# Kernel optimization log

Measured on AMD Instinct MI355X. Metric: run time of the kernel, lower is better.

The kernel has to match this reference:

```python
import jax, jax.numpy as jnp
import numpy as np

EPS = 1e-6

def ln_fwd(x, gamma, beta):
    # gamma/beta broadcast shape [1,H,1,D]
    mu = x.mean(axis=-1, keepdims=True)
    var = ((x - mu) ** 2).mean(axis=-1, keepdims=True)
    x_hat = (x - mu) / jnp.sqrt(var + EPS)
    return gamma * x_hat + beta

def ln_fused_l2_bwd(x, residual, pred, gamma, beta):
    # grad wrt x of || (gamma*ln(x)+beta) + residual - pred ||^2 (fused form)
    mu = x.mean(axis=-1, keepdims=True)
    var = ((x - mu) ** 2).mean(axis=-1, keepdims=True)
    std = jnp.sqrt(var + EPS)
    x_hat = (x - mu) / std
    y = gamma * x_hat + beta + residual
    grad_output = 2.0 * (y - pred)
    gxh = grad_output * gamma
    z = (gxh - gxh.mean(axis=-1, keepdims=True)
         - x_hat * (gxh * x_hat).mean(axis=-1, keepdims=True)) / std
    return z

def _combine(a, b):
    # a precedes b in sequence; recurrence x[t] = g[t]*x[t-1] + u[t]
    ga, ua = a
    gb, ub = b
    return (ga * gb, gb * ua + ub)

def setup_inputs() -> dict:
    key = jax.random.key(0)
    ks = jax.random.split(key, 8)
    B, H, L, D = 1, 16, 2048, 64
    q = jax.random.normal(ks[0], (B, H, L, D), dtype=jnp.float32)
    k = jax.random.normal(ks[1], (B, H, L, D), dtype=jnp.float32)
    v = jax.random.normal(ks[2], (B, H, L, D), dtype=jnp.float32)
    gate = jax.random.uniform(ks[3], (B, H, L), dtype=jnp.float32)
    eta = jax.random.uniform(ks[4], (B, H, L), dtype=jnp.float32) * 0.1
    W0 = jax.random.normal(ks[5], (H, D, D), dtype=jnp.float32) / jnp.sqrt(jnp.float32(D))
    gamma = jnp.ones((H, 1, D), dtype=jnp.float32)
    beta = jnp.zeros((H, 1, D), dtype=jnp.float32)
    return {"q": q, "k": k, "v": v, "gate": gate, "eta": eta,
            "W0": W0, "gamma": gamma, "beta": beta}

def reference(q, k, v, gate, eta, W0, gamma, beta):
    # q,k,v: [B,H,L,D]; gate,eta: [B,H,L]; W0: [H,D,D]; gamma,beta: [H,1,D]
    g = gamma[None]          # [1,H,1,D]
    b = beta[None]
    # inner-loop TTT gradient at initial fast weights W0
    Z1 = jnp.einsum('bhld,hde->bhle', k, W0)                  # [B,H,L,D]
    grad_l = ln_fused_l2_bwd(Z1, k, v, g, b)                  # [B,H,L,D]
    # per-token fast-weight update: -eta[t] * outer(k[t], grad_l[t])
    token = -eta[..., None, None] * (k[..., :, None] * grad_l[..., None, :])  # [B,H,L,D,D]
    gates = gate[..., None, None]                             # [B,H,L,1,1]
    # gated linear recurrence W[t] = gate[t]*W[t-1] + token[t] via associative scan
    gc, uc = jax.lax.associative_scan(_combine, (gates, token), axis=2)
    W = uc + gc * W0[None, :, None]                           # [B,H,L,D,D]
    # readout with post-LN and residual
    Zq = jnp.einsum('bhld,bhlde->bhle', q, W)                 # [B,H,L,D]
    out = ln_fwd(Zq, g, b) + q
    return out
```

## Files before the change

### kernel.cpp

```cpp
#include <hip/hip_runtime.h>
#include <hip/hip_bf16.h>
#include <math.h>


#define H 16
#define L 2048
#define D 64
#define C 64
#define NC 32

typedef short s8v __attribute__((ext_vector_type(8)));
typedef short s4v __attribute__((ext_vector_type(4)));
typedef float f4v __attribute__((ext_vector_type(4)));

__device__ inline unsigned short f2bf(float x) {
  unsigned u = __float_as_uint(x);
  return (unsigned short)((u + 0x7fffu + ((u >> 16) & 1u)) >> 16);
}
__device__ inline float bf2f(unsigned short s) { return __uint_as_float(((unsigned)s) << 16); }

__device__ inline int swz(int row, int colByte) { return row * 128 + (colByte ^ ((row & 7) << 4)); }

__device__ inline s8v ld8(const short* base, int row, int colByte) {
  return *(const s8v*)((const char*)base + swz(row, colByte));
}
__device__ inline void st4(short* base, int row, int colByte, s4v v) {
  *(s4v*)((char*)base + swz(row, colByte)) = v;
}
__device__ inline void st2(short* base, int row, int colByte, unsigned v) {
  *(unsigned*)((char*)base + swz(row, colByte)) = v;
}
__device__ inline void st1(short* base, int row, int colByte, unsigned short v) {
  *(short*)((char*)base + swz(row, colByte)) = (short)v;
}

__device__ inline void red16(float& x) {
  x += __shfl_xor(x, 1, 64);
  x += __shfl_xor(x, 2, 64);
  x += __shfl_xor(x, 4, 64);
  x += __shfl_xor(x, 8, 64);
}

__device__ inline f4v MM(s8v a, s8v b, f4v c) {
  return __builtin_amdgcn_mfma_f32_16x16x32_bf16(a, b, c, 0, 0, 0);
}

__device__ inline f4v MM3(s8v ah, s8v al, s8v bh, s8v bl, f4v c) {
  c = MM(ah, bh, c);
  c = MM(ah, bl, c);
  c = MM(al, bh, c);
  return c;
}

__global__ __launch_bounds__(256, 2) void k_chunk(
    const float4* __restrict__ Q4, const float4* __restrict__ K4,
    const float* __restrict__ Kg, const float* __restrict__ Vg,
    const float* __restrict__ gate, const float* __restrict__ eta,
    const float4* __restrict__ W04, const float* __restrict__ gamma,
    const float* __restrict__ beta,
    float* __restrict__ Ut, float* __restrict__ Pg, float* __restrict__ Out)
{
  __shared__ __align__(16) short Khi[4096];
  __shared__ __align__(16) short Klo[4096];
  __shared__ __align__(16) short KtH[4096];
  __shared__ __align__(16) short KtL[4096];
  __shared__ __align__(16) short W0h[4096];
  __shared__ __align__(16) short W0l[4096];
  __shared__ float cl[64], wj[64];

  int tid = threadIdx.x;
  int h = blockIdx.x >> 5, c = blockIdx.x & 31;
  int rowb = h * L + c * C;
  int R = tid >> 6, l = tid & 63, g = l >> 4, c16 = l & 15;
  int arow = 16 * R + c16;
  int kb0 = 16 * g, kb1 = 64 + 16 * g;

  const float4* qp = Q4 + (size_t)(rowb + arow) * 16;
  float4 qA0 = qp[2 * g], qA1 = qp[2 * g + 1], qA2 = qp[8 + 2 * g], qA3 = qp[8 + 2 * g + 1];
  float kk[4][4], vv[4][4], er[4];
  #pragma unroll
  for (int r = 0; r < 4; ++r) {
    int jr = 16 * R + 4 * g + r;
    const float* kp = Kg + (size_t)(rowb + jr) * 64 + c16;
    const float* vp = Vg + (size_t)(rowb + jr) * 64 + c16;
    #pragma unroll
    for (int ct = 0; ct < 4; ++ct) {
      kk[r][ct] = kp[16 * ct];
      vv[r][ct] = vp[16 * ct];
    }
    er[r] = eta[rowb + jr];
  }

  {
    float x = logf(fmaxf(gate[rowb + l], 1e-37f));
    #pragma unroll
    for (int off = 1; off < 64; off <<= 1) {
      float n = __shfl_up(x, off, 64);
      if (l >= off) x += n;
    }
    cl[l] = x;
    float c63 = __shfl(x, 63, 64);
    wj[l] = expf(c63 - x);
    if (R == 0) Pg[rowb + l] = expf(x);
  }

  #pragma unroll
  for (int it = 0; it < 2; ++it) {
    int idx = tid + it * 256;
    int rp = idx >> 4, g4 = idx & 15;
    int j0 = 2 * rp, j1 = j0 + 1;
    float4 k0 = K4[(size_t)(rowb + j0) * 16 + g4];
    float4 k1 = K4[(size_t)(rowb + j1) * 16 + g4];
    float4 w0 = W04[(size_t)h * 1024 + j0 * 16 + g4];
    float4 w1 = W04[(size_t)h * 1024 + j1 * 16 + g4];
    float w0j = wj[j0], w1j = wj[j1];
    float ke0[4] = {k0.x, k0.y, k0.z, k0.w};
    float ke1[4] = {k1.x, k1.y, k1.z, k1.w};
    float we0[4] = {w0.x, w0.y, w0.z, w0.w};
    float we1[4] = {w1.x, w1.y, w1.z, w1.w};
    s4v kh0, kl0, kh1, kl1;
    #pragma unroll
    for (int e = 0; e < 4; ++e) {
      unsigned short hb0 = f2bf(ke0[e]);
      kh0[e] = (short)hb0; kl0[e] = (short)f2bf(ke0[e] - bf2f(hb0));
      unsigned short hb1 = f2bf(ke1[e]);
      kh1[e] = (short)hb1; kl1[e] = (short)f2bf(ke1[e] - bf2f(hb1));
      int dr = 4 * g4 + e;
      float wk0 = ke0[e] * w0j, wk1 = ke1[e] * w1j;
      unsigned short th0 = f2bf(wk0), th1 = f2bf(wk1);
      st2(KtH, dr, 2 * j0, (unsigned)th0 | ((unsigned)th1 << 16));
      st2(KtL, dr, 2 * j0,
          (unsigned)f2bf(wk0 - bf2f(th0)) | ((unsigned)f2bf(wk1 - bf2f(th1)) << 16));
      unsigned short wh0 = f2bf(we0[e]), wh1 = f2bf(we1[e]);
      st2(W0h, dr, 2 * j0, (unsigned)wh0 | ((unsigned)wh1 << 16));
      st2(W0l, dr, 2 * j0,
          (unsigned)f2bf(we0[e] - bf2f(wh0)) | ((unsigned)f2bf(we1[e] - bf2f(wh1)) << 16));
    }
    st4(Khi, j0, 8 * g4, kh0); st4(Klo, j0, 8 * g4, kl0);
    st4(Khi, j1, 8 * g4, kh1); st4(Klo, j1, 8 * g4, kl1);
  }

  s8v aQh0, aQl0, aQh1, aQl1;
  {
    float q0[8] = {qA0.x, qA0.y, qA0.z, qA0.w, qA1.x, qA1.y, qA1.z, qA1.w};
    float q1[8] = {qA2.x, qA2.y, qA2.z, qA2.w, qA3.x, qA3.y, qA3.z, qA3.w};
    #pragma unroll
    for (int e = 0; e < 8; ++e) {
      unsigned short hb = f2bf(q0[e]);
      aQh0[e] = (short)hb; aQl0[e] = (short)f2bf(q0[e] - bf2f(hb));
      unsigned short hb1 = f2bf(q1[e]);
      aQh1[e] = (short)hb1; aQl1[e] = (short)f2bf(q1[e] - bf2f(hb1));
    }
  }
  __syncthreads();

  f4v accS[4];
  #pragma unroll
  for (int ct = 0; ct < 4; ++ct) {
    int br = 16 * ct + c16;
    f4v a = {0.f, 0.f, 0.f, 0.f};
    a = MM3(aQh0, aQl0, ld8(Khi, br, kb0), ld8(Klo, br, kb0), a);
    a = MM3(aQh1, aQl1, ld8(Khi, br, kb1), ld8(Klo, br, kb1), a);
    accS[ct] = a;
  }

  s8v aKh0 = ld8(Khi, arow, kb0), aKh1 = ld8(Khi, arow, kb1);
  s8v aKl0 = ld8(Klo, arow, kb0), aKl1 = ld8(Klo, arow, kb1);
  f4v accZ[4];
  #pragma unroll
  for (int ct = 0; ct < 4; ++ct) {
    int br = 16 * ct + c16;
    f4v a = {0.f, 0.f, 0.f, 0.f};
    a = MM3(aKh0, aKl0, ld8(W0h, br, kb0), ld8(W0l, br, kb0), a);
    a = MM3(aKh1, aKl1, ld8(W0h, br, kb1), ld8(W0l, br, kb1), a);
    accZ[ct] = a;
  }

  float ga[4], be[4];
  #pragma unroll
  for (int ct = 0; ct < 4; ++ct) {
    ga[ct] = gamma[h * 64 + 16 * ct + c16];
    be[ct] = beta[h * 64 + 16 * ct + c16];
  }
  float gtreg[4][4];
  #pragma unroll
  for (int r = 0; r < 4; ++r) {
    float s1 = accZ[0][r] + accZ[1][r] + accZ[2][r] + accZ[3][r];
    red16(s1);
    float mu = s1 * (1.f / 64.f);
    float dv[4], s2 = 0.f;
    #pragma unroll
    for (int ct = 0; ct < 4; ++ct) { dv[ct] = accZ[ct][r] - mu; s2 += dv[ct] * dv[ct]; }
    red16(s2);
    float rstd = rsqrtf(s2 * (1.f / 64.f) + 1e-6f);
    float xh[4], gxh[4], t1 = 0.f, t2 = 0.f;
    #pragma unroll
    for (int ct = 0; ct < 4; ++ct) {
      xh[ct] = dv[ct] * rstd;
      float go = 2.f * (fmaf(ga[ct], xh[ct], be[ct]) + kk[r][ct] - vv[r][ct]);
      gxh[ct] = go * ga[ct];
      t1 += gxh[ct];
      t2 += gxh[ct] * xh[ct];
    }
    red16(t1);
    red16(t2);
    float m1 = t1 * (1.f / 64.f), m2 = t2 * (1.f / 64.f);
    #pragma unroll
    for (int ct = 0; ct < 4; ++ct)
      gtreg[r][ct] = -er[r] * (gxh[ct] - m1 - xh[ct] * m2) * rstd;
  }
  __syncthreads();

  #pragma unroll
  for (int ct = 0; ct < 4; ++ct) {
    s4v gh, gl;
    #pragma unroll
    for (int r = 0; r < 4; ++r) {
      unsigned short hb = f2bf(gtreg[r][ct]);
      gh[r] = (short)hb;
      gl[r] = (short)f2bf(gtreg[r][ct] - bf2f(hb));
    }
    st4(W0h, 16 * ct + c16, 2 * (16 * R + 4 * g), gh);
    st4(W0l, 16 * ct + c16, 2 * (16 * R + 4 * g), gl);
  }
  float cli[4];
  #pragma unroll
  for (int r = 0; r < 4; ++r) cli[r] = cl[16 * R + 4 * g + r];
  #pragma unroll
  for (int ct = 0; ct < 4; ++ct) {
    int j = 16 * ct + c16;
    float clj = cl[j];
    #pragma unroll
    for (int r = 0; r < 4; ++r) {
      int i = 16 * R + 4 * g + r;
      float s = (j <= i) ? accS[ct][r] * expf(cli[r] - clj) : 0.f;
      unsigned short hb = f2bf(s);
      st1(Khi, i, 2 * j, hb);
      st1(Klo, i, 2 * j, f2bf(s - bf2f(hb)));
    }
  }
  __syncthreads();

  s8v aSh0 = ld8(Khi, arow, kb0), aSh1 = ld8(Khi, arow, kb1);
  s8v aSl0 = ld8(Klo, arow, kb0), aSl1 = ld8(Klo, arow, kb1);
  #pragma unroll
  for (int ct = 0; ct < 4; ++ct) {
    int br = 16 * ct + c16;
    f4v a = {0.f, 0.f, 0.f, 0.f};
    a = MM3(aSh0, aSl0, ld8(W0h, br, kb0), ld8(W0l, br, kb0), a);
    a = MM3(aSh1, aSl1, ld8(W0h, br, kb1), ld8(W0l, br, kb1), a);
    #pragma unroll
    for (int r = 0; r < 4; ++r)
      Out[(size_t)(rowb + 16 * R + 4 * g + r) * 64 + 16 * ct + c16] = a[r];
  }

  float* ub = Ut + (size_t)(h * NC + c) * 4096;
  s8v aGh0 = ld8(W0h, arow, kb0), aGh1 = ld8(W0h, arow, kb1);
  s8v aGl0 = ld8(W0l, arow, kb0), aGl1 = ld8(W0l, arow, kb1);
  #pragma unroll
  for (int ct = 0; ct < 4; ++ct) {
    int br = 16 * ct + c16;
    f4v a = {0.f, 0.f, 0.f, 0.f};
    a = MM3(aGh0, aGl0, ld8(KtH, br, kb0), ld8(KtL, br, kb0), a);
    a = MM3(aGh1, aGl1, ld8(KtH, br, kb1), ld8(KtL, br, kb1), a);
    #pragma unroll
    for (int r = 0; r < 4; ++r)
      ub[(16 * R + 4 * g + r) * 64 + 16 * ct + c16] = a[r];
  }
}

__global__ __launch_bounds__(256) void k_scan(
    const float* __restrict__ W0, const float* __restrict__ Ut,
    const float* __restrict__ Pg, float* __restrict__ Wpt)
{
  int t = blockIdx.x * 256 + threadIdx.x;
  int h = t >> 12;
  int idx = t & 4095;
  int erow = idx >> 6, d = idx & 63;
  float w = W0[h * 4096 + d * 64 + erow];
  #pragma unroll
  for (int c2 = 0; c2 < NC; ++c2) {
    int off = (h * NC + c2) * 4096 + idx;
    Wpt[off] = w;
    w = fmaf(Pg[h * L + c2 * 64 + 63], w, Ut[off]);
  }
}

__global__ __launch_bounds__(256, 2) void k_out(
    const float4* __restrict__ Q4, const float* __restrict__ Qg,
    const float4* __restrict__ Wpt4, const float* __restrict__ Pg,
    const float* __restrict__ gamma, const float* __restrict__ beta,
    float* __restrict__ Out)
{
  __shared__ __align__(16) short Whi[4096];
  __shared__ __align__(16) short Wlo[4096];
  int tid = threadIdx.x;
  int h = blockIdx.x >> 5, c = blockIdx.x & 31;
  int rowb = h * L + c * C;
  int R = tid >> 6, l = tid & 63, g = l >> 4, c16 = l & 15;
  int arow = 16 * R + c16;
  int kb0 = 16 * g, kb1 = 64 + 16 * g;

  const float4* qp = Q4 + (size_t)(rowb + arow) * 16;
  float4 qA0 = qp[2 * g], qA1 = qp[2 * g + 1], qA2 = qp[8 + 2 * g], qA3 = qp[8 + 2 * g + 1];
  float io[4][4], qres[4][4], pr[4];
  #pragma unroll
  for (int r = 0; r < 4; ++r) {
    int row = rowb + 16 * R + 4 * g + r;
    pr[r] = Pg[row];
    #pragma unroll
    for (int ct = 0; ct < 4; ++ct) {
      io[r][ct] = Out[(size_t)row * 64 + 16 * ct + c16];
      qres[r][ct] = Qg[(size_t)row * 64 + 16 * ct + c16];
    }
  }

  for (int idx = tid; idx < 1024; idx += 256) {
    int row = idx >> 4, g4 = idx & 15;
    float4 wv = Wpt4[(size_t)(h * NC + c) * 1024 + idx];
    float we[4] = {wv.x, wv.y, wv.z, wv.w};
    s4v wh, wl;
    #pragma unroll
    for (int e = 0; e < 4; ++e) {
      unsigned short hb = f2bf(we[e]);
      wh[e] = (short)hb;
      wl[e] = (short)f2bf(we[e] - bf2f(hb));
    }
    st4(Whi, row, 8 * g4, wh);
    st4(Wlo, row, 8 * g4, wl);
  }

  s8v ah0, al0, ah1, al1;
  {
    float q0[8] = {qA0.x, qA0.y, qA0.z, qA0.w, qA1.x, qA1.y, qA1.z, qA1.w};
    float q1[8] = {qA2.x, qA2.y, qA2.z, qA2.w, qA3.x, qA3.y, qA3.z, qA3.w};
    #pragma unroll
    for (int e = 0; e < 8; ++e) {
      unsigned short hb = f2bf(q0[e]);
      ah0[e] = (short)hb; al0[e] = (short)f2bf(q0[e] - bf2f(hb));
      unsigned short hb1 = f2bf(q1[e]);
      ah1[e] = (short)hb1; al1[e] = (short)f2bf(q1[e] - bf2f(hb1));
    }
  }
  __syncthreads();

  f4v acc[4];
  #pragma unroll
  for (int ct = 0; ct < 4; ++ct) {
    int br = 16 * ct + c16;
    f4v a = {0.f, 0.f, 0.f, 0.f};
    a = MM3(ah0, al0, ld8(Whi, br, kb0), ld8(Wlo, br, kb0), a);
    a = MM3(ah1, al1, ld8(Whi, br, kb1), ld8(Wlo, br, kb1), a);
    acc[ct] = a;
  }
  float ga[4], be[4];
  #pragma unroll
  for (int ct = 0; ct < 4; ++ct) {
    ga[ct] = gamma[h * 64 + 16 * ct + c16];
    be[ct] = beta[h * 64 + 16 * ct + c16];
  }
  #pragma unroll
  for (int r = 0; r < 4; ++r) {
    int row = rowb + 16 * R + 4 * g + r;
    float zq[4];
    #pragma unroll
    for (int ct = 0; ct < 4; ++ct)
      zq[ct] = fmaf(pr[r], acc[ct][r], io[r][ct]);
    float s1 = zq[0] + zq[1] + zq[2] + zq[3];
    red16(s1);
    float mu = s1 * (1.f / 64.f);
    float dv[4], s2 = 0.f;
    #pragma unroll
    for (int ct = 0; ct < 4; ++ct) { dv[ct] = zq[ct] - mu; s2 += dv[ct] * dv[ct]; }
    red16(s2);
    float rstd = rsqrtf(s2 * (1.f / 64.f) + 1e-6f);
    #pragma unroll
    for (int ct = 0; ct < 4; ++ct) {
      float o = fmaf(ga[ct], dv[ct] * rstd, be[ct]) + qres[r][ct];
      Out[(size_t)row * 64 + 16 * ct + c16] = o;
    }
  }
}

extern "C" void kernel_launch(void* const* d_in, const int* in_sizes, int n_in,
                              void* d_out, int out_size, void* d_ws, size_t ws_size,
                              hipStream_t stream) {
  const float* q     = (const float*)d_in[0];
  const float* k     = (const float*)d_in[1];
  const float* v     = (const float*)d_in[2];
  const float* gate  = (const float*)d_in[3];
  const float* eta   = (const float*)d_in[4];
  const float* W0    = (const float*)d_in[5];
  const float* gamma = (const float*)d_in[6];
  const float* beta  = (const float*)d_in[7];
  float* out = (float*)d_out;
  float* ws  = (float*)d_ws;

  float* Pg  = ws;
  float* Ut  = ws + 32768;
  float* Wpt = ws + 32768 + 2097152;

  k_chunk<<<H * NC, 256, 0, stream>>>(
      (const float4*)q, (const float4*)k, k, v, gate, eta,
      (const float4*)W0, gamma, beta, Ut, Pg, out);
  k_scan<<<256, 256, 0, stream>>>(W0, Ut, Pg, Wpt);
  k_out<<<H * NC, 256, 0, stream>>>(
      (const float4*)q, q, (const float4*)Wpt, Pg, gamma, beta, out);
}
```

Measured before the change: 31.87 us.

## Fuse chunk-state scan into chunk kernel via last-block atomic counter

Removes the separate k_scan launch. Each chunk block now increments a per-head atomic counter, and the last block for a head runs the sequential inter-chunk scan over Ut using float4 accesses. It also moves the decay weighting from the K^T operand onto the gradient operand, which needs extra LDS buffers, and issues the K/W0 global loads earlier. The trade is one fewer kernel launch against a memset launch, a serialized scan done by only 16 blocks (one per head), and higher LDS use that may reduce occupancy.

```diff
diff --git a/kernel.cpp b/kernel.cpp
--- a/kernel.cpp
+++ b/kernel.cpp
@@ -6,7 +6,6 @@
 #define H 16
 #define L 2048
 #define D 64
-#define C 64
 #define NC 32
 
 typedef short s8v __attribute__((ext_vector_type(8)));
@@ -44,7 +43,6 @@
 __device__ inline f4v MM(s8v a, s8v b, f4v c) {
   return __builtin_amdgcn_mfma_f32_16x16x32_bf16(a, b, c, 0, 0, 0);
 }
-
 __device__ inline f4v MM3(s8v ah, s8v al, s8v bh, s8v bl, f4v c) {
   c = MM(ah, bh, c);
   c = MM(ah, bl, c);
@@ -57,8 +55,9 @@
     const float* __restrict__ Kg, const float* __restrict__ Vg,
     const float* __restrict__ gate, const float* __restrict__ eta,
     const float4* __restrict__ W04, const float* __restrict__ gamma,
-    const float* __restrict__ beta,
-    float* __restrict__ Ut, float* __restrict__ Pg, float* __restrict__ Out)
+    const float* __restrict__ beta, const float* __restrict__ W0f,
+    float* __restrict__ Ut, float* __restrict__ Pg, float* __restrict__ Gc,
+    float* __restrict__ Wpt, int* __restrict__ Cnt, float* __restrict__ Out)
 {
   __shared__ __align__(16) short Khi[4096];
   __shared__ __align__(16) short Klo[4096];
@@ -66,14 +65,31 @@
   __shared__ __align__(16) short KtL[4096];
   __shared__ __align__(16) short W0h[4096];
   __shared__ __align__(16) short W0l[4096];
-  __shared__ float cl[64], wj[64];
+  __shared__ __align__(16) short GwH[4096];
+  __shared__ __align__(16) short GwL[4096];
+  __shared__ float cl[64];
+  __shared__ int lastFlag;
 
   int tid = threadIdx.x;
-  int h = blockIdx.x >> 5, c = blockIdx.x & 31;
-  int rowb = h * L + c * C;
+  int bid = blockIdx.x;
+  int h = bid >> 5;
+  int rowb = h * L + (bid & 31) * 64;
   int R = tid >> 6, l = tid & 63, g = l >> 4, c16 = l & 15;
   int arow = 16 * R + c16;
   int kb0 = 16 * g, kb1 = 64 + 16 * g;
+
+  float gv = gate[rowb + l];
+
+  int g4 = tid & 15;
+  float4 kA[2][2], wA[2][2];
+  #pragma unroll
+  for (int it = 0; it < 2; ++it) {
+    int j0 = 2 * ((tid >> 4) + it * 16);
+    kA[it][0] = K4[(size_t)(rowb + j0) * 16 + g4];
+    kA[it][1] = K4[(size_t)(rowb + j0 + 1) * 16 + g4];
+    wA[it][0] = W04[(size_t)h * 1024 + j0 * 16 + g4];
+    wA[it][1] = W04[(size_t)h * 1024 + (j0 + 1) * 16 + g4];
+  }
 
   const float4* qp = Q4 + (size_t)(rowb + arow) * 16;
   float4 qA0 = qp[2 * g], qA1 = qp[2 * g + 1], qA2 = qp[8 + 2 * g], qA3 = qp[8 + 2 * g + 1];
@@ -91,53 +107,46 @@
     er[r] = eta[rowb + jr];
   }
 
+  float c63v;
   {
-    float x = logf(fmaxf(gate[rowb + l], 1e-37f));
+    float x = logf(fmaxf(gv, 1e-37f));
     #pragma unroll
     for (int off = 1; off < 64; off <<= 1) {
       float n = __shfl_up(x, off, 64);
       if (l >= off) x += n;
     }
     cl[l] = x;
-    float c63 = __shfl(x, 63, 64);
-    wj[l] = expf(c63 - x);
+    c63v = __shfl(x, 63, 64);
     if (R == 0) Pg[rowb + l] = expf(x);
+    if (tid == 63) Gc[bid] = expf(x);
   }
 
   #pragma unroll
   for (int it = 0; it < 2; ++it) {
-    int idx = tid + it * 256;
-    int rp = idx >> 4, g4 = idx & 15;
-    int j0 = 2 * rp, j1 = j0 + 1;
-    float4 k0 = K4[(size_t)(rowb + j0) * 16 + g4];
-    float4 k1 = K4[(size_t)(rowb + j1) * 16 + g4];
-    float4 w0 = W04[(size_t)h * 1024 + j0 * 16 + g4];
-    float4 w1 = W04[(size_t)h * 1024 + j1 * 16 + g4];
-    float w0j = wj[j0], w1j = wj[j1];
-    float ke0[4] = {k0.x, k0.y, k0.z, k0.w};
-    float ke1[4] = {k1.x, k1.y, k1.z, k1.w};
-    float we0[4] = {w0.x, w0.y, w0.z, w0.w};
-    float we1[4] = {w1.x, w1.y, w1.z, w1.w};
+    int j0 = 2 * ((tid >> 4) + it * 16);
+    float ke0[4] = {kA[it][0].x, kA[it][0].y, kA[it][0].z, kA[it][0].w};
+    float ke1[4] = {kA[it][1].x, kA[it][1].y, kA[it][1].z, kA[it][1].w};
+    float we0[4] = {wA[it][0].x, wA[it][0].y, wA[it][0].z, wA[it][0].w};
+    float we1[4] = {wA[it][1].x, wA[it][1].y, wA[it][1].z, wA[it][1].w};
     s4v kh0, kl0, kh1, kl1;
     #pragma unroll
     for (int e = 0; e < 4; ++e) {
       unsigned short hb0 = f2bf(ke0[e]);
-      kh0[e] = (short)hb0; kl0[e] = (short)f2bf(ke0[e] - bf2f(hb0));
+      unsigned short lb0 = f2bf(ke0[e] - bf2f(hb0));
       unsigned short hb1 = f2bf(ke1[e]);
-      kh1[e] = (short)hb1; kl1[e] = (short)f2bf(ke1[e] - bf2f(hb1));
+      unsigned short lb1 = f2bf(ke1[e] - bf2f(hb1));
+      kh0[e] = (short)hb0; kl0[e] = (short)lb0;
+      kh1[e] = (short)hb1; kl1[e] = (short)lb1;
       int dr = 4 * g4 + e;
-      float wk0 = ke0[e] * w0j, wk1 = ke1[e] * w1j;
-      unsigned short th0 = f2bf(wk0), th1 = f2bf(wk1);
-      st2(KtH, dr, 2 * j0, (unsigned)th0 | ((unsigned)th1 << 16));
-      st2(KtL, dr, 2 * j0,
-          (unsigned)f2bf(wk0 - bf2f(th0)) | ((unsigned)f2bf(wk1 - bf2f(th1)) << 16));
+      st2(KtH, dr, 2 * j0, (unsigned)hb0 | ((unsigned)hb1 << 16));
+      st2(KtL, dr, 2 * j0, (unsigned)lb0 | ((unsigned)lb1 << 16));
       unsigned short wh0 = f2bf(we0[e]), wh1 = f2bf(we1[e]);
       st2(W0h, dr, 2 * j0, (unsigned)wh0 | ((unsigned)wh1 << 16));
       st2(W0l, dr, 2 * j0,
           (unsigned)f2bf(we0[e] - bf2f(wh0)) | ((unsigned)f2bf(we1[e] - bf2f(wh1)) << 16));
     }
     st4(Khi, j0, 8 * g4, kh0); st4(Klo, j0, 8 * g4, kl0);
-    st4(Khi, j1, 8 * g4, kh1); st4(Klo, j1, 8 * g4, kl1);
+    st4(Khi, j0 + 1, 8 * g4, kh1); st4(Klo, j0 + 1, 8 * g4, kl1);
   }
 
   s8v aQh0, aQl0, aQh1, aQl1;
@@ -181,6 +190,12 @@
   for (int ct = 0; ct < 4; ++ct) {
     ga[ct] = gamma[h * 64 + 16 * ct + c16];
     be[ct] = beta[h * 64 + 16 * ct + c16];
+  }
+  float cli[4], wjr[4];
+  #pragma unroll
+  for (int r = 0; r < 4; ++r) {
+    cli[r] = cl[16 * R + 4 * g + r];
+    wjr[r] = expf(c63v - cli[r]);
   }
   float gtreg[4][4];
   #pragma unroll
@@ -213,19 +228,22 @@
 
   #pragma unroll
   for (int ct = 0; ct < 4; ++ct) {
-    s4v gh, gl;
+    s4v gh, gl, uh, ul;
     #pragma unroll
     for (int r = 0; r < 4; ++r) {
-      unsigned short hb = f2bf(gtreg[r][ct]);
+      float gtv = gtreg[r][ct];
+      unsigned short hb = f2bf(gtv);
       gh[r] = (short)hb;
-      gl[r] = (short)f2bf(gtreg[r][ct] - bf2f(hb));
-    }
-    st4(W0h, 16 * ct + c16, 2 * (16 * R + 4 * g), gh);
-    st4(W0l, 16 * ct + c16, 2 * (16 * R + 4 * g), gl);
-  }
-  float cli[4];
-  #pragma unroll
-  for (int r = 0; r < 4; ++r) cli[r] = cl[16 * R + 4 * g + r];
+      gl[r] = (short)f2bf(gtv - bf2f(hb));
+      float gw = gtv * wjr[r];
+      unsigned short hb2 = f2bf(gw);
+      uh[r] = (short)hb2;
+      ul[r] = (short)f2bf(gw - bf2f(hb2));
+    }
+    int er2 = 16 * ct + c16, cb = 2 * (16 * R + 4 * g);
+    st4(W0h, er2, cb, gh); st4(W0l, er2, cb, gl);
+    st4(GwH, er2, cb, uh); st4(GwL, er2, cb, ul);
+  }
   #pragma unroll
   for (int ct = 0; ct < 4; ++ct) {
     int j = 16 * ct + c16;
@@ -254,9 +272,9 @@
       Out[(size_t)(rowb + 16 * R + 4 * g + r) * 64 + 16 * ct + c16] = a[r];
   }
 
-  float* ub = Ut + (size_t)(h * NC + c) * 4096;
-  s8v aGh0 = ld8(W0h, arow, kb0), aGh1 = ld8(W0h, arow, kb1);
-  s8v aGl0 = ld8(W0l, arow, kb0), aGl1 = ld8(W0l, arow, kb1);
+  float* ub = Ut + (size_t)bid * 4096;
+  s8v aGh0 = ld8(GwH, arow, kb0), aGh1 = ld8(GwH, arow, kb1);
+  s8v aGl0 = ld8(GwL, arow, kb0), aGl1 = ld8(GwL, arow, kb1);
   #pragma unroll
   for (int ct = 0; ct < 4; ++ct) {
     int br = 16 * ct + c16;
@@ -267,22 +285,42 @@
     for (int r = 0; r < 4; ++r)
       ub[(16 * R + 4 * g + r) * 64 + 16 * ct + c16] = a[r];
   }
-}
-
-__global__ __launch_bounds__(256) void k_scan(
-    const float* __restrict__ W0, const float* __restrict__ Ut,
-    const float* __restrict__ Pg, float* __restrict__ Wpt)
-{
-  int t = blockIdx.x * 256 + threadIdx.x;
-  int h = t >> 12;
-  int idx = t & 4095;
-  int erow = idx >> 6, d = idx & 63;
-  float w = W0[h * 4096 + d * 64 + erow];
-  #pragma unroll
-  for (int c2 = 0; c2 < NC; ++c2) {
-    int off = (h * NC + c2) * 4096 + idx;
-    Wpt[off] = w;
-    w = fmaf(Pg[h * L + c2 * 64 + 63], w, Ut[off]);
+
+  __syncthreads();
+  if (tid == 0) {
+    __threadfence();
+    lastFlag = (atomicAdd(&Cnt[h], 1) == NC - 1) ? 1 : 0;
+  }
+  __syncthreads();
+  if (lastFlag) {
+    __threadfence();
+    const float4* ut4 = (const float4*)Ut + (size_t)h * NC * 1024;
+    float4* wp4 = (float4*)Wpt + (size_t)h * NC * 1024;
+    const float* gcp = Gc + h * NC;
+    float4 w[4];
+    #pragma unroll
+    for (int j = 0; j < 4; ++j) {
+      int e4 = tid + j * 256;
+      int erow = e4 >> 4, d0 = (e4 & 15) * 4;
+      const float* w0p = W0f + (size_t)h * 4096 + erow;
+      w[j].x = w0p[(d0 + 0) * 64];
+      w[j].y = w0p[(d0 + 1) * 64];
+      w[j].z = w0p[(d0 + 2) * 64];
+      w[j].w = w0p[(d0 + 3) * 64];
+    }
+    for (int c2 = 0; c2 < NC; ++c2) {
+      float gcv = gcp[c2];
+      #pragma unroll
+      for (int j = 0; j < 4; ++j) {
+        size_t off = (size_t)c2 * 1024 + tid + j * 256;
+        wp4[off] = w[j];
+        float4 u = ut4[off];
+        w[j].x = fmaf(gcv, w[j].x, u.x);
+        w[j].y = fmaf(gcv, w[j].y, u.y);
+        w[j].z = fmaf(gcv, w[j].z, u.z);
+        w[j].w = fmaf(gcv, w[j].w, u.w);
+      }
+    }
   }
 }
 
@@ -296,7 +334,7 @@
   __shared__ __align__(16) short Wlo[4096];
   int tid = threadIdx.x;
   int h = blockIdx.x >> 5, c = blockIdx.x & 31;
-  int rowb = h * L + c * C;
+  int rowb = h * L + c * 64;
   int R = tid >> 6, l = tid & 63, g = l >> 4, c16 = l & 15;
   int arow = 16 * R + c16;
   int kb0 = 16 * g, kb1 = 64 + 16 * g;
@@ -397,13 +435,16 @@
   float* ws  = (float*)d_ws;
 
   float* Pg  = ws;
-  float* Ut  = ws + 32768;
-  float* Wpt = ws + 32768 + 2097152;
-
+  float* Gc  = ws + 32768;
+  float* Ut  = ws + 33280;
+  float* Wpt = ws + 33280 + 2097152;
+  int*   Cnt = (int*)(ws + 33280 + 2 * 2097152);
+
+  hipMemsetAsync(Cnt, 0, H * sizeof(int), stream);
   k_chunk<<<H * NC, 256, 0, stream>>>(
       (const float4*)q, (const float4*)k, k, v, gate, eta,
-      (const float4*)W0, gamma, beta, Ut, Pg, out);
-  k_scan<<<256, 256, 0, stream>>>(W0, Ut, Pg, Wpt);
+      (const float4*)W0, gamma, beta, W0,
+      Ut, Pg, Gc, Wpt, Cnt, out);
   k_out<<<H * NC, 256, 0, stream>>>(
       (const float4*)q, q, (const float4*)Wpt, Pg, gamma, beta, out);
 }
```

Result: slower. 78.20 us (+145.4%).

## Split chunk and output kernels across 8 waves with column-halved tiles

Applied to the files above, without the earlier changes.

Doubles the block size of k_chunk and k_out to 512 threads. Each pair of waves splits the 64 output columns, and the row statistics for the layer norms are exchanged through shared memory. The decay weighting now multiplies the gradient tile into separate GwH/GwL buffers instead of scaling K during staging, and the variance uses E[x^2]-mu^2 in a single pass. The aim is more waves in flight and shorter per-wave dependency chains, at the cost of extra barriers, more LDS, and a slightly less stable variance formula.

```diff
diff --git a/kernel.cpp b/kernel.cpp
--- a/kernel.cpp
+++ b/kernel.cpp
@@ -6,7 +6,6 @@
 #define H 16
 #define L 2048
 #define D 64
-#define C 64
 #define NC 32
 
 typedef short s8v __attribute__((ext_vector_type(8)));
@@ -44,7 +43,6 @@
 __device__ inline f4v MM(s8v a, s8v b, f4v c) {
   return __builtin_amdgcn_mfma_f32_16x16x32_bf16(a, b, c, 0, 0, 0);
 }
-
 __device__ inline f4v MM3(s8v ah, s8v al, s8v bh, s8v bl, f4v c) {
   c = MM(ah, bh, c);
   c = MM(ah, bl, c);
@@ -52,7 +50,7 @@
   return c;
 }
 
-__global__ __launch_bounds__(256, 2) void k_chunk(
+__global__ __launch_bounds__(512, 4) void k_chunk(
     const float4* __restrict__ Q4, const float4* __restrict__ K4,
     const float* __restrict__ Kg, const float* __restrict__ Vg,
     const float* __restrict__ gate, const float* __restrict__ eta,
@@ -66,71 +64,75 @@
   __shared__ __align__(16) short KtL[4096];
   __shared__ __align__(16) short W0h[4096];
   __shared__ __align__(16) short W0l[4096];
-  __shared__ float cl[64], wj[64];
+  __shared__ __align__(16) short GwH[4096];
+  __shared__ __align__(16) short GwL[4096];
+  __shared__ float cl[64];
+  __shared__ float exA[2][64], exB[2][64], exC[2][64], exD[2][64];
 
   int tid = threadIdx.x;
-  int h = blockIdx.x >> 5, c = blockIdx.x & 31;
-  int rowb = h * L + c * C;
-  int R = tid >> 6, l = tid & 63, g = l >> 4, c16 = l & 15;
-  int arow = 16 * R + c16;
+  int h = blockIdx.x >> 5;
+  int rowb = h * L + (blockIdx.x & 31) * 64;
+  int w = tid >> 6, l = tid & 63;
+  int RG = w >> 1, CH = w & 1;
+  int g = l >> 4, c16 = l & 15;
+  int arow = 16 * RG + c16;
   int kb0 = 16 * g, kb1 = 64 + 16 * g;
+
+  float gv = gate[rowb + l];
+
+  int pairI = tid >> 4, g4 = tid & 15;
+  int j0 = 2 * pairI, j1 = j0 + 1;
+  float4 kA0 = K4[(size_t)(rowb + j0) * 16 + g4];
+  float4 kA1 = K4[(size_t)(rowb + j1) * 16 + g4];
+  float4 wA0 = W04[(size_t)h * 1024 + j0 * 16 + g4];
+  float4 wA1 = W04[(size_t)h * 1024 + j1 * 16 + g4];
 
   const float4* qp = Q4 + (size_t)(rowb + arow) * 16;
   float4 qA0 = qp[2 * g], qA1 = qp[2 * g + 1], qA2 = qp[8 + 2 * g], qA3 = qp[8 + 2 * g + 1];
-  float kk[4][4], vv[4][4], er[4];
-  #pragma unroll
-  for (int r = 0; r < 4; ++r) {
-    int jr = 16 * R + 4 * g + r;
+  float kk[4][2], vv[4][2], er[4];
+  #pragma unroll
+  for (int r = 0; r < 4; ++r) {
+    int jr = 16 * RG + 4 * g + r;
     const float* kp = Kg + (size_t)(rowb + jr) * 64 + c16;
     const float* vp = Vg + (size_t)(rowb + jr) * 64 + c16;
     #pragma unroll
-    for (int ct = 0; ct < 4; ++ct) {
-      kk[r][ct] = kp[16 * ct];
-      vv[r][ct] = vp[16 * ct];
+    for (int j = 0; j < 2; ++j) {
+      kk[r][j] = kp[16 * (2 * CH + j)];
+      vv[r][j] = vp[16 * (2 * CH + j)];
     }
     er[r] = eta[rowb + jr];
   }
 
+  float c63v;
   {
-    float x = logf(fmaxf(gate[rowb + l], 1e-37f));
+    float x = logf(fmaxf(gv, 1e-37f));
     #pragma unroll
     for (int off = 1; off < 64; off <<= 1) {
       float n = __shfl_up(x, off, 64);
       if (l >= off) x += n;
     }
     cl[l] = x;
-    float c63 = __shfl(x, 63, 64);
-    wj[l] = expf(c63 - x);
-    if (R == 0) Pg[rowb + l] = expf(x);
-  }
-
-  #pragma unroll
-  for (int it = 0; it < 2; ++it) {
-    int idx = tid + it * 256;
-    int rp = idx >> 4, g4 = idx & 15;
-    int j0 = 2 * rp, j1 = j0 + 1;
-    float4 k0 = K4[(size_t)(rowb + j0) * 16 + g4];
-    float4 k1 = K4[(size_t)(rowb + j1) * 16 + g4];
-    float4 w0 = W04[(size_t)h * 1024 + j0 * 16 + g4];
-    float4 w1 = W04[(size_t)h * 1024 + j1 * 16 + g4];
-    float w0j = wj[j0], w1j = wj[j1];
-    float ke0[4] = {k0.x, k0.y, k0.z, k0.w};
-    float ke1[4] = {k1.x, k1.y, k1.z, k1.w};
-    float we0[4] = {w0.x, w0.y, w0.z, w0.w};
-    float we1[4] = {w1.x, w1.y, w1.z, w1.w};
+    c63v = __shfl(x, 63, 64);
+    if (w == 0) Pg[rowb + l] = expf(x);
+  }
+
+  {
+    float ke0[4] = {kA0.x, kA0.y, kA0.z, kA0.w};
+    float ke1[4] = {kA1.x, kA1.y, kA1.z, kA1.w};
+    float we0[4] = {wA0.x, wA0.y, wA0.z, wA0.w};
+    float we1[4] = {wA1.x, wA1.y, wA1.z, wA1.w};
     s4v kh0, kl0, kh1, kl1;
     #pragma unroll
     for (int e = 0; e < 4; ++e) {
       unsigned short hb0 = f2bf(ke0[e]);
-      kh0[e] = (short)hb0; kl0[e] = (short)f2bf(ke0[e] - bf2f(hb0));
+      unsigned short lb0 = f2bf(ke0[e] - bf2f(hb0));
       unsigned short hb1 = f2bf(ke1[e]);
-      kh1[e] = (short)hb1; kl1[e] = (short)f2bf(ke1[e] - bf2f(hb1));
+      unsigned short lb1 = f2bf(ke1[e] - bf2f(hb1));
+      kh0[e] = (short)hb0; kl0[e] = (short)lb0;
+      kh1[e] = (short)hb1; kl1[e] = (short)lb1;
       int dr = 4 * g4 + e;
-      float wk0 = ke0[e] * w0j, wk1 = ke1[e] * w1j;
-      unsigned short th0 = f2bf(wk0), th1 = f2bf(wk1);
-      st2(KtH, dr, 2 * j0, (unsigned)th0 | ((unsigned)th1 << 16));
-      st2(KtL, dr, 2 * j0,
-          (unsigned)f2bf(wk0 - bf2f(th0)) | ((unsigned)f2bf(wk1 - bf2f(th1)) << 16));
+      st2(KtH, dr, 2 * j0, (unsigned)hb0 | ((unsigned)hb1 << 16));
+      st2(KtL, dr, 2 * j0, (unsigned)lb0 | ((unsigned)lb1 << 16));
       unsigned short wh0 = f2bf(we0[e]), wh1 = f2bf(we1[e]);
       st2(W0h, dr, 2 * j0, (unsigned)wh0 | ((unsigned)wh1 << 16));
       st2(W0l, dr, 2 * j0,
@@ -154,89 +156,114 @@
   }
   __syncthreads();
 
-  f4v accS[4];
-  #pragma unroll
-  for (int ct = 0; ct < 4; ++ct) {
-    int br = 16 * ct + c16;
+  f4v accS[2];
+  #pragma unroll
+  for (int ct2 = 0; ct2 < 2; ++ct2) {
+    int br = 16 * (2 * CH + ct2) + c16;
     f4v a = {0.f, 0.f, 0.f, 0.f};
     a = MM3(aQh0, aQl0, ld8(Khi, br, kb0), ld8(Klo, br, kb0), a);
     a = MM3(aQh1, aQl1, ld8(Khi, br, kb1), ld8(Klo, br, kb1), a);
-    accS[ct] = a;
+    accS[ct2] = a;
   }
 
   s8v aKh0 = ld8(Khi, arow, kb0), aKh1 = ld8(Khi, arow, kb1);
   s8v aKl0 = ld8(Klo, arow, kb0), aKl1 = ld8(Klo, arow, kb1);
-  f4v accZ[4];
-  #pragma unroll
-  for (int ct = 0; ct < 4; ++ct) {
-    int br = 16 * ct + c16;
+  f4v accZ[2];
+  #pragma unroll
+  for (int ct2 = 0; ct2 < 2; ++ct2) {
+    int br = 16 * (2 * CH + ct2) + c16;
     f4v a = {0.f, 0.f, 0.f, 0.f};
     a = MM3(aKh0, aKl0, ld8(W0h, br, kb0), ld8(W0l, br, kb0), a);
     a = MM3(aKh1, aKl1, ld8(W0h, br, kb1), ld8(W0l, br, kb1), a);
-    accZ[ct] = a;
-  }
-
-  float ga[4], be[4];
-  #pragma unroll
-  for (int ct = 0; ct < 4; ++ct) {
-    ga[ct] = gamma[h * 64 + 16 * ct + c16];
-    be[ct] = beta[h * 64 + 16 * ct + c16];
-  }
-  float gtreg[4][4];
-  #pragma unroll
-  for (int r = 0; r < 4; ++r) {
-    float s1 = accZ[0][r] + accZ[1][r] + accZ[2][r] + accZ[3][r];
-    red16(s1);
-    float mu = s1 * (1.f / 64.f);
-    float dv[4], s2 = 0.f;
-    #pragma unroll
-    for (int ct = 0; ct < 4; ++ct) { dv[ct] = accZ[ct][r] - mu; s2 += dv[ct] * dv[ct]; }
-    red16(s2);
-    float rstd = rsqrtf(s2 * (1.f / 64.f) + 1e-6f);
-    float xh[4], gxh[4], t1 = 0.f, t2 = 0.f;
-    #pragma unroll
-    for (int ct = 0; ct < 4; ++ct) {
-      xh[ct] = dv[ct] * rstd;
-      float go = 2.f * (fmaf(ga[ct], xh[ct], be[ct]) + kk[r][ct] - vv[r][ct]);
-      gxh[ct] = go * ga[ct];
-      t1 += gxh[ct];
-      t2 += gxh[ct] * xh[ct];
+    accZ[ct2] = a;
+  }
+
+  float ga2[2], be2[2];
+  #pragma unroll
+  for (int j = 0; j < 2; ++j) {
+    ga2[j] = gamma[h * 64 + 16 * (2 * CH + j) + c16];
+    be2[j] = beta[h * 64 + 16 * (2 * CH + j) + c16];
+  }
+  float cli[4], wjr[4];
+  #pragma unroll
+  for (int r = 0; r < 4; ++r) {
+    cli[r] = cl[16 * RG + 4 * g + r];
+    wjr[r] = expf(c63v - cli[r]);
+  }
+  #pragma unroll
+  for (int r = 0; r < 4; ++r) {
+    int jr = 16 * RG + 4 * g + r;
+    float z0 = accZ[0][r], z1 = accZ[1][r];
+    float p1 = z0 + z1;
+    float p2 = z0 * z0 + z1 * z1;
+    red16(p1);
+    red16(p2);
+    if (c16 == 0) { exA[CH][jr] = p1; exB[CH][jr] = p2; }
+  }
+  __syncthreads();
+  float mu[4], rs[4], xh[4][2], gxh[4][2];
+  #pragma unroll
+  for (int r = 0; r < 4; ++r) {
+    int jr = 16 * RG + 4 * g + r;
+    float s1 = exA[0][jr] + exA[1][jr];
+    float sq = exB[0][jr] + exB[1][jr];
+    mu[r] = s1 * (1.f / 64.f);
+    float var = sq * (1.f / 64.f) - mu[r] * mu[r];
+    rs[r] = rsqrtf(var + 1e-6f);
+    float t1 = 0.f, t2 = 0.f;
+    #pragma unroll
+    for (int j = 0; j < 2; ++j) {
+      xh[r][j] = (accZ[j][r] - mu[r]) * rs[r];
+      float go = 2.f * (fmaf(ga2[j], xh[r][j], be2[j]) + kk[r][j] - vv[r][j]);
+      gxh[r][j] = go * ga2[j];
+      t1 += gxh[r][j];
+      t2 += gxh[r][j] * xh[r][j];
     }
     red16(t1);
     red16(t2);
-    float m1 = t1 * (1.f / 64.f), m2 = t2 * (1.f / 64.f);
-    #pragma unroll
-    for (int ct = 0; ct < 4; ++ct)
-      gtreg[r][ct] = -er[r] * (gxh[ct] - m1 - xh[ct] * m2) * rstd;
-  }
-  __syncthreads();
-
-  #pragma unroll
-  for (int ct = 0; ct < 4; ++ct) {
-    s4v gh, gl;
+    if (c16 == 0) { exC[CH][jr] = t1; exD[CH][jr] = t2; }
+  }
+  __syncthreads();
+  float gtreg[4][2];
+  #pragma unroll
+  for (int r = 0; r < 4; ++r) {
+    int jr = 16 * RG + 4 * g + r;
+    float m1 = (exC[0][jr] + exC[1][jr]) * (1.f / 64.f);
+    float m2 = (exD[0][jr] + exD[1][jr]) * (1.f / 64.f);
+    #pragma unroll
+    for (int j = 0; j < 2; ++j)
+      gtreg[r][j] = -er[r] * (gxh[r][j] - m1 - xh[r][j] * m2) * rs[r];
+  }
+
+  #pragma unroll
+  for (int j = 0; j < 2; ++j) {
+    s4v gh, gl, uh, ul;
     #pragma unroll
     for (int r = 0; r < 4; ++r) {
-      unsigned short hb = f2bf(gtreg[r][ct]);
+      float gtv = gtreg[r][j];
+      unsigned short hb = f2bf(gtv);
       gh[r] = (short)hb;
-      gl[r] = (short)f2bf(gtreg[r][ct] - bf2f(hb));
-    }
-    st4(W0h, 16 * ct + c16, 2 * (16 * R + 4 * g), gh);
-    st4(W0l, 16 * ct + c16, 2 * (16 * R + 4 * g), gl);
-  }
-  float cli[4];
-  #pragma unroll
-  for (int r = 0; r < 4; ++r) cli[r] = cl[16 * R + 4 * g + r];
-  #pragma unroll
-  for (int ct = 0; ct < 4; ++ct) {
-    int j = 16 * ct + c16;
-    float clj = cl[j];
+      gl[r] = (short)f2bf(gtv - bf2f(hb));
+      float gw = gtv * wjr[r];
+      unsigned short hb2 = f2bf(gw);
+      uh[r] = (short)hb2;
+      ul[r] = (short)f2bf(gw - bf2f(hb2));
+    }
+    int er2 = 16 * (2 * CH + j) + c16, cb = 2 * (16 * RG + 4 * g);
+    st4(W0h, er2, cb, gh); st4(W0l, er2, cb, gl);
+    st4(GwH, er2, cb, uh); st4(GwL, er2, cb, ul);
+  }
+  #pragma unroll
+  for (int j = 0; j < 2; ++j) {
+    int jj = 16 * (2 * CH + j) + c16;
+    float clj = cl[jj];
     #pragma unroll
     for (int r = 0; r < 4; ++r) {
-      int i = 16 * R + 4 * g + r;
-      float s = (j <= i) ? accS[ct][r] * expf(cli[r] - clj) : 0.f;
+      int i = 16 * RG + 4 * g + r;
+      float s = (jj <= i) ? accS[j][r] * expf(cli[r] - clj) : 0.f;
       unsigned short hb = f2bf(s);
-      st1(Khi, i, 2 * j, hb);
-      st1(Klo, i, 2 * j, f2bf(s - bf2f(hb)));
+      st1(Khi, i, 2 * jj, hb);
+      st1(Klo, i, 2 * jj, f2bf(s - bf2f(hb)));
     }
   }
   __syncthreads();
@@ -244,28 +271,28 @@
   s8v aSh0 = ld8(Khi, arow, kb0), aSh1 = ld8(Khi, arow, kb1);
   s8v aSl0 = ld8(Klo, arow, kb0), aSl1 = ld8(Klo, arow, kb1);
   #pragma unroll
-  for (int ct = 0; ct < 4; ++ct) {
-    int br = 16 * ct + c16;
+  for (int ct2 = 0; ct2 < 2; ++ct2) {
+    int br = 16 * (2 * CH + ct2) + c16;
     f4v a = {0.f, 0.f, 0.f, 0.f};
     a = MM3(aSh0, aSl0, ld8(W0h, br, kb0), ld8(W0l, br, kb0), a);
     a = MM3(aSh1, aSl1, ld8(W0h, br, kb1), ld8(W0l, br, kb1), a);
     #pragma unroll
     for (int r = 0; r < 4; ++r)
-      Out[(size_t)(rowb + 16 * R + 4 * g + r) * 64 + 16 * ct + c16] = a[r];
-  }
-
-  float* ub = Ut + (size_t)(h * NC + c) * 4096;
-  s8v aGh0 = ld8(W0h, arow, kb0), aGh1 = ld8(W0h, arow, kb1);
-  s8v aGl0 = ld8(W0l, arow, kb0), aGl1 = ld8(W0l, arow, kb1);
-  #pragma unroll
-  for (int ct = 0; ct < 4; ++ct) {
-    int br = 16 * ct + c16;
+      Out[(size_t)(rowb + 16 * RG + 4 * g + r) * 64 + br] = a[r];
+  }
+
+  float* ub = Ut + (size_t)blockIdx.x * 4096;
+  s8v aGh0 = ld8(GwH, arow, kb0), aGh1 = ld8(GwH, arow, kb1);
+  s8v aGl0 = ld8(GwL, arow, kb0), aGl1 = ld8(GwL, arow, kb1);
+  #pragma unroll
+  for (int ct2 = 0; ct2 < 2; ++ct2) {
+    int br = 16 * (2 * CH + ct2) + c16;
     f4v a = {0.f, 0.f, 0.f, 0.f};
     a = MM3(aGh0, aGl0, ld8(KtH, br, kb0), ld8(KtL, br, kb0), a);
     a = MM3(aGh1, aGl1, ld8(KtH, br, kb1), ld8(KtL, br, kb1), a);
     #pragma unroll
     for (int r = 0; r < 4; ++r)
-      ub[(16 * R + 4 * g + r) * 64 + 16 * ct + c16] = a[r];
+      ub[(16 * RG + 4 * g + r) * 64 + br] = a[r];
   }
 }
 
@@ -286,7 +313,7 @@
   }
 }
 
-__global__ __launch_bounds__(256, 2) void k_out(
+__global__ __launch_bounds__(512, 4) void k_out(
     const float4* __restrict__ Q4, const float* __restrict__ Qg,
     const float4* __restrict__ Wpt4, const float* __restrict__ Pg,
     const float* __restrict__ gamma, const float* __restrict__ beta,
@@ -294,40 +321,50 @@
 {
   __shared__ __align__(16) short Whi[4096];
   __shared__ __align__(16) short Wlo[4096];
+  __shared__ float exA[2][64], exB[2][64];
   int tid = threadIdx.x;
-  int h = blockIdx.x >> 5, c = blockIdx.x & 31;
-  int rowb = h * L + c * C;
-  int R = tid >> 6, l = tid & 63, g = l >> 4, c16 = l & 15;
-  int arow = 16 * R + c16;
+  int h = blockIdx.x >> 5;
+  int rowb = h * L + (blockIdx.x & 31) * 64;
+  int w = tid >> 6, l = tid & 63;
+  int RG = w >> 1, CH = w & 1;
+  int g = l >> 4, c16 = l & 15;
+  int arow = 16 * RG + c16;
   int kb0 = 16 * g, kb1 = 64 + 16 * g;
+
+  float4 wv0 = Wpt4[(size_t)blockIdx.x * 1024 + tid];
+  float4 wv1 = Wpt4[(size_t)blockIdx.x * 1024 + tid + 512];
 
   const float4* qp = Q4 + (size_t)(rowb + arow) * 16;
   float4 qA0 = qp[2 * g], qA1 = qp[2 * g + 1], qA2 = qp[8 + 2 * g], qA3 = qp[8 + 2 * g + 1];
-  float io[4][4], qres[4][4], pr[4];
-  #pragma unroll
-  for (int r = 0; r < 4; ++r) {
-    int row = rowb + 16 * R + 4 * g + r;
+  float io[4][2], qres[4][2], pr[4];
+  #pragma unroll
+  for (int r = 0; r < 4; ++r) {
+    int row = rowb + 16 * RG + 4 * g + r;
     pr[r] = Pg[row];
     #pragma unroll
-    for (int ct = 0; ct < 4; ++ct) {
-      io[r][ct] = Out[(size_t)row * 64 + 16 * ct + c16];
-      qres[r][ct] = Qg[(size_t)row * 64 + 16 * ct + c16];
-    }
-  }
-
-  for (int idx = tid; idx < 1024; idx += 256) {
-    int row = idx >> 4, g4 = idx & 15;
-    float4 wv = Wpt4[(size_t)(h * NC + c) * 1024 + idx];
-    float we[4] = {wv.x, wv.y, wv.z, wv.w};
-    s4v wh, wl;
+    for (int j = 0; j < 2; ++j) {
+      int col = 16 * (2 * CH + j) + c16;
+      io[r][j] = Out[(size_t)row * 64 + col];
+      qres[r][j] = Qg[(size_t)row * 64 + col];
+    }
+  }
+
+  {
+    int idx0 = tid, idx1 = tid + 512;
+    float we0[4] = {wv0.x, wv0.y, wv0.z, wv0.w};
+    float we1[4] = {wv1.x, wv1.y, wv1.z, wv1.w};
+    s4v wh0, wl0, wh1, wl1;
     #pragma unroll
     for (int e = 0; e < 4; ++e) {
-      unsigned short hb = f2bf(we[e]);
-      wh[e] = (short)hb;
-      wl[e] = (short)f2bf(we[e] - bf2f(hb));
-    }
-    st4(Whi, row, 8 * g4, wh);
-    st4(Wlo, row, 8 * g4, wl);
+      unsigned short hb0 = f2bf(we0[e]);
+      wh0[e] = (short)hb0; wl0[e] = (short)f2bf(we0[e] - bf2f(hb0));
+      unsigned short hb1 = f2bf(we1[e]);
+      wh1[e] = (short)hb1; wl1[e] = (short)f2bf(we1[e] - bf2f(hb1));
+    }
+    st4(Whi, idx0 >> 4, 8 * (idx0 & 15), wh0);
+    st4(Wlo, idx0 >> 4, 8 * (idx0 & 15), wl0);
+    st4(Whi, idx1 >> 4, 8 * (idx1 & 15), wh1);
+    st4(Wlo, idx1 >> 4, 8 * (idx1 & 15), wl1);
   }
 
   s8v ah0, al0, ah1, al1;
@@ -344,40 +381,52 @@
   }
   __syncthreads();
 
-  f4v acc[4];
-  #pragma unroll
-  for (int ct = 0; ct < 4; ++ct) {
-    int br = 16 * ct + c16;
+  f4v acc[2];
+  #pragma unroll
+  for (int ct2 = 0; ct2 < 2; ++ct2) {
+    int br = 16 * (2 * CH + ct2) + c16;
     f4v a = {0.f, 0.f, 0.f, 0.f};
     a = MM3(ah0, al0, ld8(Whi, br, kb0), ld8(Wlo, br, kb0), a);
     a = MM3(ah1, al1, ld8(Whi, br, kb1), ld8(Wlo, br, kb1), a);
-    acc[ct] = a;
-  }
-  float ga[4], be[4];
-  #pragma unroll
-  for (int ct = 0; ct < 4; ++ct) {
-    ga[ct] = gamma[h * 64 + 16 * ct + c16];
-    be[ct] = beta[h * 64 + 16 * ct + c16];
-  }
-  #pragma unroll
-  for (int r = 0; r < 4; ++r) {
-    int row = rowb + 16 * R + 4 * g + r;
-    float zq[4];
-    #pragma unroll
-    for (int ct = 0; ct < 4; ++ct)
-      zq[ct] = fmaf(pr[r], acc[ct][r], io[r][ct]);
-    float s1 = zq[0] + zq[1] + zq[2] + zq[3];
-    red16(s1);
+    acc[ct2] = a;
+  }
+
+  float zq[4][2];
+  #pragma unroll
+  for (int r = 0; r < 4; ++r) {
+    int jr = 16 * RG + 4 * g + r;
+    float p1 = 0.f, p2 = 0.f;
+    #pragma unroll
+    for (int j = 0; j < 2; ++j) {
+      zq[r][j] = fmaf(pr[r], acc[j][r], io[r][j]);
+      p1 += zq[r][j];
+      p2 += zq[r][j] * zq[r][j];
+    }
+    red16(p1);
+    red16(p2);
+    if (c16 == 0) { exA[CH][jr] = p1; exB[CH][jr] = p2; }
+  }
+  __syncthreads();
+  float ga2[2], be2[2];
+  #pragma unroll
+  for (int j = 0; j < 2; ++j) {
+    ga2[j] = gamma[h * 64 + 16 * (2 * CH + j) + c16];
+    be2[j] = beta[h * 64 + 16 * (2 * CH + j) + c16];
+  }
+  #pragma unroll
+  for (int r = 0; r < 4; ++r) {
+    int jr = 16 * RG + 4 * g + r;
+    int row = rowb + jr;
+    float s1 = exA[0][jr] + exA[1][jr];
+    float sq = exB[0][jr] + exB[1][jr];
     float mu = s1 * (1.f / 64.f);
-    float dv[4], s2 = 0.f;
-    #pragma unroll
-    for (int ct = 0; ct < 4; ++ct) { dv[ct] = zq[ct] - mu; s2 += dv[ct] * dv[ct]; }
-    red16(s2);
-    float rstd = rsqrtf(s2 * (1.f / 64.f) + 1e-6f);
-    #pragma unroll
-    for (int ct = 0; ct < 4; ++ct) {
-      float o = fmaf(ga[ct], dv[ct] * rstd, be[ct]) + qres[r][ct];
-      Out[(size_t)row * 64 + 16 * ct + c16] = o;
+    float var = sq * (1.f / 64.f) - mu * mu;
+    float rstd = rsqrtf(var + 1e-6f);
+    #pragma unroll
+    for (int j = 0; j < 2; ++j) {
+      int col = 16 * (2 * CH + j) + c16;
+      float o = fmaf(ga2[j], (zq[r][j] - mu) * rstd, be2[j]) + qres[r][j];
+      Out[(size_t)row * 64 + col] = o;
     }
   }
 }
@@ -400,10 +449,10 @@
   float* Ut  = ws + 32768;
   float* Wpt = ws + 32768 + 2097152;
 
-  k_chunk<<<H * NC, 256, 0, stream>>>(
+  k_chunk<<<H * NC, 512, 0, stream>>>(
       (const float4*)q, (const float4*)k, k, v, gate, eta,
       (const float4*)W0, gamma, beta, Ut, Pg, out);
   k_scan<<<256, 256, 0, stream>>>(W0, Ut, Pg, Wpt);
-  k_out<<<H * NC, 256, 0, stream>>>(
+  k_out<<<H * NC, 512, 0, stream>>>(
       (const float4*)q, q, (const float4*)Wpt, Pg, gamma, beta, out);
 }
```

Result: slower. 33.28 us (+4.4%).
